# Performance work log

Hardware: AMD Instinct MI355X
Metric: run time of the kernel (lower is better)

The kernel has to match this reference:

```python
import jax, jax.numpy as jnp
import numpy as np

H, DH = 4, 32  # heads, dim_head
EPS = 1e-5


def _split_heads(t, b, n):
    # b n m (h d) -> b h n m d
    return t.reshape(b, n, n, H, DH).transpose(0, 3, 1, 2, 4)


def setup_inputs() -> dict:
    key = jax.random.key(0)
    ks = jax.random.split(key, 8)
    b, n, d = 1, 256, 128
    s = 0.02
    return {
        "edges": jax.random.normal(ks[0], (b, n, n, d), jnp.float32),
        "mask": jax.random.randint(ks[1], (b, n, n), 0, 2) > 0,
        "ln_gamma": jnp.ones((d,), jnp.float32),
        "ln_beta": jnp.zeros((d,), jnp.float32),
        "W_qkv": jax.random.normal(ks[2], (d, 3 * H * DH), jnp.float32) * s,
        "W_b": jax.random.normal(ks[3], (d, H), jnp.float32) * s,
        "W_g": jax.random.normal(ks[4], (d, H * DH), jnp.float32) * s,
        "b_g": jnp.zeros((H * DH,), jnp.float32),
        "W_out": jax.random.normal(ks[5], (H * DH, d), jnp.float32) * s,
        "b_out": jnp.zeros((d,), jnp.float32),
    }


def reference(edges, mask, ln_gamma, ln_beta, W_qkv, W_b, W_g, b_g, W_out, b_out):
    b, n = edges.shape[0], edges.shape[1]
    scale = DH ** -0.5
    # pre-norm (LayerNorm over feature dim)
    mu = edges.mean(-1, keepdims=True)
    var = ((edges - mu) ** 2).mean(-1, keepdims=True)
    x = (edges - mu) * jax.lax.rsqrt(var + EPS) * ln_gamma + ln_beta

    qkv = x @ W_qkv
    q, k, v = jnp.split(qkv, 3, axis=-1)
    q, k, v = (_split_heads(t, b, n) for t in (q, k, v))  # b h i j d
    g = _split_heads(jax.nn.sigmoid(x @ W_g + b_g), b, n)  # b h i j d
    bias = (x @ W_b).transpose(0, 3, 1, 2)  # b h j k

    # starting-node attention: keys/values share row i
    sim = jnp.einsum("bhijd,bhikd->bhijk", q, k) * scale + bias[:, :, None, :, :]
    neg = jnp.finfo(sim.dtype).min
    am = (~mask)[:, None, :, :, None]  # b 1 i j 1
    sim = jnp.where(am, neg, sim)
    g = jnp.where(am, neg, g)
    attn = jax.nn.softmax(sim, axis=-1)
    out = g * jnp.einsum("bhijk,bhikd->bhijd", attn, v)
    # b h i j d -> b i j (h d)
    out = out.transpose(0, 2, 3, 1, 4).reshape(b, n, n, H * DH)
    return out @ W_out + b_out
```

## Files before the change

kernel.cpp:

```cpp
#include <hip/hip_runtime.h>
#include <hip/hip_bf16.h>
#include <hip/hip_fp16.h>


#define NP  256
#define DD  128
#define HSTR 2097152

typedef short bf16x8 __attribute__((ext_vector_type(8)));
typedef float f32x4  __attribute__((ext_vector_type(4)));

__device__ __forceinline__ float bf2f(ushort u) {
    union { unsigned int v; float f; } c; c.v = ((unsigned int)u) << 16; return c.f;
}
__device__ __forceinline__ float asf(unsigned int v) {
    union { unsigned int v; float f; } c; c.v = v; return c.f;
}
__device__ __forceinline__ ushort f2bf(float f) {
    union { float f; unsigned int v; } c; c.f = f;
    unsigned int x = c.v;
    return (ushort)((x + 0x7FFFu + ((x >> 16) & 1u)) >> 16);
}
__device__ __forceinline__ unsigned int packbf(float a, float b) {
    __hip_bfloat162 t = __float22bfloat162_rn(make_float2(a, b));
    union { __hip_bfloat162 h; unsigned int u; } c; c.h = t; return c.u;
}
__device__ __forceinline__ f32x4 mfma16(bf16x8 a, bf16x8 b, f32x4 c) {
    return __builtin_amdgcn_mfma_f32_16x16x32_bf16(a, b, c, 0, 0, 0);
}

#define NEGV (-3.4028234663852886e38f)
#define SCALE 0.17677669529663687f

__global__ __launch_bounds__(256) void k_wconv(
    const float* __restrict__ Wqkv, const float* __restrict__ Wg,
    const float* __restrict__ Wout, const float* __restrict__ Wb,
    ushort* __restrict__ WT, ushort* __restrict__ WoT,
    ushort* __restrict__ WbT16)
{
    int idx = blockIdx.x * 256 + threadIdx.x;
    if (idx < 65536) {
        int n = idx >> 7, k = idx & 127;
        float v = (n < 384) ? Wqkv[(size_t)k * 384 + n]
                            : Wg[(size_t)k * 128 + (n - 384)];
        WT[idx] = f2bf(v);
    } else if (idx < 81920) {
        int i2 = idx - 65536;
        int c = i2 >> 7, e = i2 & 127;
        WoT[i2] = f2bf(Wout[(size_t)e * 128 + c]);
    } else {
        int i3 = idx - 81920;
        int c = i3 >> 7, e = i3 & 127;
        WbT16[i3] = (c < 4) ? f2bf(Wb[(size_t)e * 4 + c]) : (ushort)0;
    }
}

__global__ __launch_bounds__(256) void k_lnqkvg(
    const float* __restrict__ edges, const float* __restrict__ gamma,
    const float* __restrict__ beta,  const ushort* __restrict__ WbT16,
    const ushort* __restrict__ WT,   const float* __restrict__ bg,
    ushort* __restrict__ Bo16,
    ushort* __restrict__ Qo, ushort* __restrict__ Ko,
    ushort* __restrict__ Vo, ushort* __restrict__ Go)
{
    __shared__ __align__(16) ushort As[64][136];
    __shared__ __align__(16) ushort Bs[128][136];
    const int tid = threadIdx.x, w = tid >> 6, lane = tid & 63;
    const int lr = lane & 15, lg = lane >> 4;
    const int wm = w >> 1, wn = w & 1;
    const int p0 = blockIdx.x * 64;
    const f32x4 zz = {0.f, 0.f, 0.f, 0.f};

    {
        const int row = w * 16 + lr;
        const int part = lg;
        const float* ep = edges + (size_t)(p0 + row) * DD + part * 32;
        float4 xv[8];
        #pragma unroll
        for (int t = 0; t < 8; ++t)
            xv[t] = *reinterpret_cast<const float4*>(ep + t * 4);
        float s = 0.f, ss = 0.f;
        #pragma unroll
        for (int t = 0; t < 8; ++t) {
            s  += (xv[t].x + xv[t].y) + (xv[t].z + xv[t].w);
            ss += (xv[t].x * xv[t].x + xv[t].y * xv[t].y)
                + (xv[t].z * xv[t].z + xv[t].w * xv[t].w);
        }
        s  += __shfl_xor(s, 16);  s  += __shfl_xor(s, 32);
        ss += __shfl_xor(ss, 16); ss += __shfl_xor(ss, 32);
        const float mu = s * 0.0078125f;
        const float var = ss * 0.0078125f - mu * mu;
        const float rstd = rsqrtf(var + 1e-5f);
        const float* gp = gamma + part * 32;
        const float* bp = beta + part * 32;
        #pragma unroll
        for (int u = 0; u < 4; ++u) {
            float4 a = xv[2 * u], b = xv[2 * u + 1];
            float4 ga = *reinterpret_cast<const float4*>(gp + u * 8);
            float4 gb = *reinterpret_cast<const float4*>(gp + u * 8 + 4);
            float4 ba = *reinterpret_cast<const float4*>(bp + u * 8);
            float4 bb = *reinterpret_cast<const float4*>(bp + u * 8 + 4);
            float cg;
            uint4 st;
            float v0, v1;
            cg = rstd * ga.x; v0 = a.x * cg + (ba.x - mu * cg);
            cg = rstd * ga.y; v1 = a.y * cg + (ba.y - mu * cg);
            st.x = packbf(v0, v1);
            cg = rstd * ga.z; v0 = a.z * cg + (ba.z - mu * cg);
            cg = rstd * ga.w; v1 = a.w * cg + (ba.w - mu * cg);
            st.y = packbf(v0, v1);
            cg = rstd * gb.x; v0 = b.x * cg + (bb.x - mu * cg);
            cg = rstd * gb.y; v1 = b.y * cg + (bb.y - mu * cg);
            st.z = packbf(v0, v1);
            cg = rstd * gb.z; v0 = b.z * cg + (bb.z - mu * cg);
            cg = rstd * gb.w; v1 = b.w * cg + (bb.w - mu * cg);
            st.w = packbf(v0, v1);
            *reinterpret_cast<uint4*>(&As[row][part * 32 + u * 8]) = st;
        }
    }
    {
        f32x4 bacc = zz;
        #pragma unroll
        for (int kk = 0; kk < 4; ++kk) {
            bf16x8 wb = *reinterpret_cast<const bf16x8*>(&WbT16[(size_t)lr * DD + kk * 32 + lg * 8]);
            bf16x8 xf = *reinterpret_cast<const bf16x8*>(&As[w * 16 + lr][kk * 32 + lg * 8]);
            bacc = mfma16(wb, xf, bacc);
        }
        if (lg == 0) {
            const int p = p0 + w * 16 + lr;
            const int j = p >> 8, k = p & 255;
            const int fn = k >> 4, lgk = (k >> 2) & 3, rr = k & 3;
            const size_t fo = (((size_t)j * 4 + lgk) * 16 + fn) * 4 + rr;
            #pragma unroll
            for (int r = 0; r < 4; ++r)
                Bo16[(size_t)r * 65536 + fo] = f2bf(bacc[r]);
        }
    }

    for (int seg = 0; seg < 4; ++seg) {
        const int n0 = seg * 128;
        __syncthreads();
        #pragma unroll
        for (int it = 0; it < 8; ++it) {
            int idx = it * 256 + tid;
            int r = idx >> 4, c = (idx & 15) * 8;
            *reinterpret_cast<uint4*>(&Bs[r][c]) =
                *reinterpret_cast<const uint4*>(&WT[(size_t)(n0 + r) * DD + c]);
        }
        __syncthreads();
        f32x4 acc[2][4];
        #pragma unroll
        for (int m = 0; m < 2; ++m)
            #pragma unroll
            for (int n = 0; n < 4; ++n) acc[m][n] = zz;
        #pragma unroll
        for (int kk = 0; kk < 4; ++kk) {
            bf16x8 a0 = *reinterpret_cast<const bf16x8*>(&As[wm * 32 + lr][kk * 32 + lg * 8]);
            bf16x8 a1 = *reinterpret_cast<const bf16x8*>(&As[wm * 32 + 16 + lr][kk * 32 + lg * 8]);
            #pragma unroll
            for (int n = 0; n < 4; ++n) {
                bf16x8 b = *reinterpret_cast<const bf16x8*>(&Bs[wn * 64 + n * 16 + lr][kk * 32 + lg * 8]);
                acc[0][n] = mfma16(b, a0, acc[0][n]);
                acc[1][n] = mfma16(b, a1, acc[1][n]);
            }
        }
        #pragma unroll
        for (int n = 0; n < 4; ++n) {
            const int ccb = wn * 64 + n * 16 + 4 * lg;
            const int hh = (wn * 64 + n * 16) >> 5;
            const int dhb = ccb & 31;
            float4 bg4;
            if (seg == 3) bg4 = *reinterpret_cast<const float4*>(&bg[ccb]);
            #pragma unroll
            for (int m = 0; m < 2; ++m) {
                const int p = p0 + wm * 32 + m * 16 + lr;
                const size_t off = (size_t)hh * HSTR + (size_t)p * 32 + dhb;
                float v0 = acc[m][n][0], v1 = acc[m][n][1];
                float v2 = acc[m][n][2], v3 = acc[m][n][3];
                uint2 st;
                if (seg == 0) {
                    st.x = packbf(v0 * SCALE, v1 * SCALE);
                    st.y = packbf(v2 * SCALE, v3 * SCALE);
                    *reinterpret_cast<uint2*>(&Qo[off]) = st;
                } else if (seg == 1) {
                    st.x = packbf(v0, v1); st.y = packbf(v2, v3);
                    *reinterpret_cast<uint2*>(&Ko[off]) = st;
                } else if (seg == 2) {
                    st.x = packbf(v0, v1); st.y = packbf(v2, v3);
                    *reinterpret_cast<uint2*>(&Vo[off]) = st;
                } else {
                    float s0 = 1.0f / (1.0f + __expf(-(v0 + bg4.x)));
                    float s1 = 1.0f / (1.0f + __expf(-(v1 + bg4.y)));
                    float s2 = 1.0f / (1.0f + __expf(-(v2 + bg4.z)));
                    float s3 = 1.0f / (1.0f + __expf(-(v3 + bg4.w)));
                    st.x = packbf(s0, s1); st.y = packbf(s2, s3);
                    *reinterpret_cast<uint2*>(&Go[off]) = st;
                }
            }
        }
    }
}

__global__ __launch_bounds__(256, 2) void k_attn9(
    const ushort* __restrict__ Qw, const ushort* __restrict__ Kw,
    const ushort* __restrict__ Vw, const ushort* __restrict__ Bo16,
    const int* __restrict__ mask, ushort* __restrict__ OPre)
{
    __shared__ __align__(16) ushort Ks[256][40];
    __shared__ __align__(16) ushort Vt[32][268];
    const int tid = threadIdx.x, w = tid >> 6, lane = tid & 63;
    const int lr = lane & 15, lg = lane >> 4;
    const int bid = blockIdx.x;
    const int h = (bid & 7) >> 1;
    const int i = ((bid >> 3) << 1) | (bid & 1);
    const int ib = i * NP;
    const size_t base = (size_t)h * HSTR + (size_t)ib * 32;

    #pragma unroll
    for (int it = 0; it < 4; ++it) {
        int idx = it * 256 + tid;
        int r = idx >> 2, c = (idx & 3) * 8;
        *reinterpret_cast<uint4*>(&Ks[r][c]) =
            *reinterpret_cast<const uint4*>(&Kw[base + (size_t)r * 32 + c]);
    }
    #pragma unroll
    for (int it = 0; it < 8; ++it) {
        int idx = it * 256 + tid;
        int d = idx & 31, k4 = (idx >> 5) * 4;
        int kk4 = (k4 & ~31) | (((k4 >> 2) & 1) << 4) | (((k4 >> 3) & 3) << 2);
        ushort4 v;
        v.x = Vw[base + (size_t)(kk4 + 0) * 32 + d];
        v.y = Vw[base + (size_t)(kk4 + 1) * 32 + d];
        v.z = Vw[base + (size_t)(kk4 + 2) * 32 + d];
        v.w = Vw[base + (size_t)(kk4 + 3) * 32 + d];
        *reinterpret_cast<ushort4*>(&Vt[d][k4]) = v;
    }
    __syncthreads();

    const ushort* bias_h = Bo16 + (size_t)h * 65536;
    const f32x4 zz = {0.f, 0.f, 0.f, 0.f};

    for (int jt = 0; jt < 4; ++jt) {
        const int jb = jt * 64 + w * 16;
        const int jq = jb + lr;
        bf16x8 q = *reinterpret_cast<const bf16x8*>(&Qw[base + (size_t)jq * 32 + lg * 8]);
        const ushort* bp = bias_h + ((size_t)jq * 4 + lg) * 64;
        f32x4 s[16];
        #pragma unroll
        for (int u = 0; u < 8; ++u) {
            uint4 b4 = *reinterpret_cast<const uint4*>(bp + u * 8);
            f32x4 s0, s1;
            s0[0] = asf(b4.x << 16); s0[1] = asf(b4.x & 0xffff0000u);
            s0[2] = asf(b4.y << 16); s0[3] = asf(b4.y & 0xffff0000u);
            s1[0] = asf(b4.z << 16); s1[1] = asf(b4.z & 0xffff0000u);
            s1[2] = asf(b4.w << 16); s1[3] = asf(b4.w & 0xffff0000u);
            s[2 * u] = s0; s[2 * u + 1] = s1;
        }
        #pragma unroll
        for (int fn = 0; fn < 16; ++fn) {
            bf16x8 a = *reinterpret_cast<const bf16x8*>(&Ks[fn * 16 + lr][lg * 8]);
            s[fn] = mfma16(a, q, s[fn]);
        }
        float mx = -3.402823466e38f;
        #pragma unroll
        for (int fn = 0; fn < 16; ++fn) {
            float m01 = fmaxf(s[fn][0], s[fn][1]);
            float m23 = fmaxf(s[fn][2], s[fn][3]);
            mx = fmaxf(mx, fmaxf(m01, m23));
        }
        mx = fmaxf(mx, __shfl_xor(mx, 16));
        mx = fmaxf(mx, __shfl_xor(mx, 32));
        float sum = 0.f;
        #pragma unroll
        for (int fn = 0; fn < 16; ++fn) {
            #pragma unroll
            for (int r = 0; r < 4; ++r) {
                float e = __expf(s[fn][r] - mx);
                s[fn][r] = e; sum += e;
            }
        }
        sum += __shfl_xor(sum, 16);
        sum += __shfl_xor(sum, 32);
        const bool masked = (mask[ib + jq] == 0);
        const float iv = masked ? 1.0f : (1.0f / sum);

        f32x4 o0 = zz, o1 = zz;
        #pragma unroll
        for (int m = 0; m < 8; ++m) {
            union { unsigned int u[4]; bf16x8 v; } pa;
            pa.u[0] = masked ? 0x3B803B80u : packbf(s[2 * m][0], s[2 * m][1]);
            pa.u[1] = masked ? 0x3B803B80u : packbf(s[2 * m][2], s[2 * m][3]);
            pa.u[2] = masked ? 0x3B803B80u : packbf(s[2 * m + 1][0], s[2 * m + 1][1]);
            pa.u[3] = masked ? 0x3B803B80u : packbf(s[2 * m + 1][2], s[2 * m + 1][3]);
            bf16x8 v0 = *reinterpret_cast<const bf16x8*>(&Vt[lr][m * 32 + lg * 8]);
            bf16x8 v1 = *reinterpret_cast<const bf16x8*>(&Vt[16 + lr][m * 32 + lg * 8]);
            o0 = mfma16(v0, pa.v, o0);
            o1 = mfma16(v1, pa.v, o1);
        }
        const size_t off = base + (size_t)jq * 32;
        uint2 u0, u1;
        u0.x = packbf(o0[0] * iv, o0[1] * iv);
        u0.y = packbf(o0[2] * iv, o0[3] * iv);
        u1.x = packbf(o1[0] * iv, o1[1] * iv);
        u1.y = packbf(o1[2] * iv, o1[3] * iv);
        *reinterpret_cast<uint2*>(&OPre[off + 4 * lg])      = u0;
        *reinterpret_cast<uint2*>(&OPre[off + 16 + 4 * lg]) = u1;
    }
}

__device__ __forceinline__ unsigned int gate2(unsigned int o2, unsigned int g2, bool mk) {
    float a0 = bf2f((ushort)(o2 & 0xffffu)), a1 = bf2f((ushort)(o2 >> 16));
    float g0 = mk ? NEGV : bf2f((ushort)(g2 & 0xffffu));
    float g1 = mk ? NEGV : bf2f((ushort)(g2 >> 16));
    return packbf(a0 * g0, a1 * g1);
}

__global__ __launch_bounds__(256) void k_gemm_out(
    const ushort* __restrict__ OPre, const ushort* __restrict__ Gw,
    const int* __restrict__ mask, const ushort* __restrict__ WoT,
    const float* __restrict__ bout, float* __restrict__ out)
{
    __shared__ __align__(16) ushort As[64][136];
    __shared__ __align__(16) ushort Bs[128][136];
    const int tid = threadIdx.x;
    const int p0 = blockIdx.x * 64;
    #pragma unroll
    for (int it = 0; it < 4; ++it) {
        int idx = it * 256 + tid;
        int r = idx >> 4, c = (idx & 15) * 8;
        int hh = c >> 5, dq = c & 31;
        const int p = p0 + r;
        const size_t go = (size_t)hh * HSTR + (size_t)p * 32 + dq;
        uint4 ov = *reinterpret_cast<const uint4*>(&OPre[go]);
        uint4 gv = *reinterpret_cast<const uint4*>(&Gw[go]);
        const bool mk = (mask[p] == 0);
        uint4 rs;
        rs.x = gate2(ov.x, gv.x, mk);
        rs.y = gate2(ov.y, gv.y, mk);
        rs.z = gate2(ov.z, gv.z, mk);
        rs.w = gate2(ov.w, gv.w, mk);
        *reinterpret_cast<uint4*>(&As[r][c]) = rs;
    }
    #pragma unroll
    for (int it = 0; it < 8; ++it) {
        int idx = it * 256 + tid;
        int r = idx >> 4, c = (idx & 15) * 8;
        *reinterpret_cast<uint4*>(&Bs[r][c]) =
            *reinterpret_cast<const uint4*>(&WoT[(size_t)r * DD + c]);
    }
    __syncthreads();
    const int w = tid >> 6, lane = tid & 63;
    const int wm = w >> 1, wn = w & 1;
    const int lr = lane & 15, lg = lane >> 4;
    const f32x4 zz = {0.f, 0.f, 0.f, 0.f};
    f32x4 acc[2][4];
    #pragma unroll
    for (int m = 0; m < 2; ++m)
        #pragma unroll
        for (int n = 0; n < 4; ++n) acc[m][n] = zz;
    #pragma unroll
    for (int kk = 0; kk < 4; ++kk) {
        bf16x8 a0 = *reinterpret_cast<const bf16x8*>(&As[wm * 32 + lr][kk * 32 + lg * 8]);
        bf16x8 a1 = *reinterpret_cast<const bf16x8*>(&As[wm * 32 + 16 + lr][kk * 32 + lg * 8]);
        #pragma unroll
        for (int n = 0; n < 4; ++n) {
            bf16x8 b = *reinterpret_cast<const bf16x8*>(&Bs[wn * 64 + n * 16 + lr][kk * 32 + lg * 8]);
            acc[0][n] = mfma16(b, a0, acc[0][n]);
            acc[1][n] = mfma16(b, a1, acc[1][n]);
        }
    }
    #pragma unroll
    for (int n = 0; n < 4; ++n) {
        const int cb = wn * 64 + n * 16 + 4 * lg;
        const float4 bo4 = *reinterpret_cast<const float4*>(&bout[cb]);
        #pragma unroll
        for (int m = 0; m < 2; ++m) {
            const int p = p0 + wm * 32 + m * 16 + lr;
            float4 st;
            st.x = acc[m][n][0] + bo4.x;
            st.y = acc[m][n][1] + bo4.y;
            st.z = acc[m][n][2] + bo4.z;
            st.w = acc[m][n][3] + bo4.w;
            *reinterpret_cast<float4*>(&out[(size_t)p * DD + cb]) = st;
        }
    }
}

extern "C" void kernel_launch(void* const* d_in, const int* in_sizes, int n_in,
                              void* d_out, int out_size, void* d_ws, size_t ws_size,
                              hipStream_t stream) {
    const float* edges = (const float*)d_in[0];
    const int*   mask  = (const int*)d_in[1];
    const float* gamma = (const float*)d_in[2];
    const float* beta  = (const float*)d_in[3];
    const float* Wqkv  = (const float*)d_in[4];
    const float* Wb    = (const float*)d_in[5];
    const float* Wg    = (const float*)d_in[6];
    const float* bg    = (const float*)d_in[7];
    const float* Wout  = (const float*)d_in[8];
    const float* bout  = (const float*)d_in[9];
    float* out = (float*)d_out;

    char* ws = (char*)d_ws;
    ushort* OPre = (ushort*)(ws);
    ushort* Qw  = (ushort*)(ws + 1u * 16777216u);
    ushort* Kw  = (ushort*)(ws + 2u * 16777216u);
    ushort* Vw  = (ushort*)(ws + 3u * 16777216u);
    ushort* Gw  = (ushort*)(ws + 4u * 16777216u);
    ushort* Bo16 = (ushort*)(ws + 5u * 16777216u);
    ushort* WT  = (ushort*)(ws + 5u * 16777216u + 524288u);
    ushort* WoT = (ushort*)(ws + 5u * 16777216u + 524288u + 131072u);
    ushort* WbT16 = (ushort*)(ws + 5u * 16777216u + 524288u + 131072u + 32768u);

    k_wconv<<<dim3(328), dim3(256), 0, stream>>>(Wqkv, Wg, Wout, Wb, WT, WoT, WbT16);
    k_lnqkvg<<<dim3(1024), dim3(256), 0, stream>>>(edges, gamma, beta, WbT16, WT, bg,
                                                   Bo16, Qw, Kw, Vw, Gw);
    k_attn9<<<dim3(1024), dim3(256), 0, stream>>>(Qw, Kw, Vw, Bo16, mask, OPre);
    k_gemm_out<<<dim3(1024), dim3(256), 0, stream>>>(OPre, Gw, mask, WoT, bout, out);
}
```

Measured before the change: 92.10 us.

## Fuse gating into attention kernel and widen attention blocks to 512 threads

Moves the sigmoid-gate multiply and mask handling from the output GEMM's A-tile load into the attention epilogue. The GEMM then reads the already-gated attention output directly, dropping a full read of the gate tensor and the mask there. The attention kernel now uses 512-thread blocks with 8 waves, fewer loop iterations and a simpler block-to-(head,row) mapping. This adds gate loads and register pressure to the attention kernel and changes occupancy bounds.

```diff
diff --git a/kernel.cpp b/kernel.cpp
--- a/kernel.cpp
+++ b/kernel.cpp
@@ -201,9 +201,10 @@
     }
 }
 
-__global__ __launch_bounds__(256, 2) void k_attn9(
+__global__ __launch_bounds__(512, 4) void k_attn10(
     const ushort* __restrict__ Qw, const ushort* __restrict__ Kw,
-    const ushort* __restrict__ Vw, const ushort* __restrict__ Bo16,
+    const ushort* __restrict__ Vw, const ushort* __restrict__ Gw,
+    const ushort* __restrict__ Bo16,
     const int* __restrict__ mask, ushort* __restrict__ OPre)
 {
     __shared__ __align__(16) ushort Ks[256][40];
@@ -211,21 +212,21 @@
     const int tid = threadIdx.x, w = tid >> 6, lane = tid & 63;
     const int lr = lane & 15, lg = lane >> 4;
     const int bid = blockIdx.x;
-    const int h = (bid & 7) >> 1;
-    const int i = ((bid >> 3) << 1) | (bid & 1);
+    const int h = bid & 3;
+    const int i = bid >> 2;
     const int ib = i * NP;
     const size_t base = (size_t)h * HSTR + (size_t)ib * 32;
 
     #pragma unroll
-    for (int it = 0; it < 4; ++it) {
-        int idx = it * 256 + tid;
+    for (int it = 0; it < 2; ++it) {
+        int idx = it * 512 + tid;
         int r = idx >> 2, c = (idx & 3) * 8;
         *reinterpret_cast<uint4*>(&Ks[r][c]) =
             *reinterpret_cast<const uint4*>(&Kw[base + (size_t)r * 32 + c]);
     }
     #pragma unroll
-    for (int it = 0; it < 8; ++it) {
-        int idx = it * 256 + tid;
+    for (int it = 0; it < 4; ++it) {
+        int idx = it * 512 + tid;
         int d = idx & 31, k4 = (idx >> 5) * 4;
         int kk4 = (k4 & ~31) | (((k4 >> 2) & 1) << 4) | (((k4 >> 3) & 3) << 2);
         ushort4 v;
@@ -240,8 +241,9 @@
     const ushort* bias_h = Bo16 + (size_t)h * 65536;
     const f32x4 zz = {0.f, 0.f, 0.f, 0.f};
 
-    for (int jt = 0; jt < 4; ++jt) {
-        const int jb = jt * 64 + w * 16;
+    #pragma unroll
+    for (int jt = 0; jt < 2; ++jt) {
+        const int jb = jt * 128 + w * 16;
         const int jq = jb + lr;
         bf16x8 q = *reinterpret_cast<const bf16x8*>(&Qw[base + (size_t)jq * 32 + lg * 8]);
         const ushort* bp = bias_h + ((size_t)jq * 4 + lg) * 64;
@@ -298,26 +300,28 @@
             o1 = mfma16(v1, pa.v, o1);
         }
         const size_t off = base + (size_t)jq * 32;
+        uint2 gv0 = *reinterpret_cast<const uint2*>(&Gw[off + 4 * lg]);
+        uint2 gv1 = *reinterpret_cast<const uint2*>(&Gw[off + 16 + 4 * lg]);
+        float g0 = masked ? NEGV : bf2f((ushort)(gv0.x & 0xffffu));
+        float g1 = masked ? NEGV : bf2f((ushort)(gv0.x >> 16));
+        float g2 = masked ? NEGV : bf2f((ushort)(gv0.y & 0xffffu));
+        float g3 = masked ? NEGV : bf2f((ushort)(gv0.y >> 16));
+        float g4 = masked ? NEGV : bf2f((ushort)(gv1.x & 0xffffu));
+        float g5 = masked ? NEGV : bf2f((ushort)(gv1.x >> 16));
+        float g6 = masked ? NEGV : bf2f((ushort)(gv1.y & 0xffffu));
+        float g7 = masked ? NEGV : bf2f((ushort)(gv1.y >> 16));
         uint2 u0, u1;
-        u0.x = packbf(o0[0] * iv, o0[1] * iv);
-        u0.y = packbf(o0[2] * iv, o0[3] * iv);
-        u1.x = packbf(o1[0] * iv, o1[1] * iv);
-        u1.y = packbf(o1[2] * iv, o1[3] * iv);
+        u0.x = packbf(o0[0] * iv * g0, o0[1] * iv * g1);
+        u0.y = packbf(o0[2] * iv * g2, o0[3] * iv * g3);
+        u1.x = packbf(o1[0] * iv * g4, o1[1] * iv * g5);
+        u1.y = packbf(o1[2] * iv * g6, o1[3] * iv * g7);
         *reinterpret_cast<uint2*>(&OPre[off + 4 * lg])      = u0;
         *reinterpret_cast<uint2*>(&OPre[off + 16 + 4 * lg]) = u1;
     }
 }
 
-__device__ __forceinline__ unsigned int gate2(unsigned int o2, unsigned int g2, bool mk) {
-    float a0 = bf2f((ushort)(o2 & 0xffffu)), a1 = bf2f((ushort)(o2 >> 16));
-    float g0 = mk ? NEGV : bf2f((ushort)(g2 & 0xffffu));
-    float g1 = mk ? NEGV : bf2f((ushort)(g2 >> 16));
-    return packbf(a0 * g0, a1 * g1);
-}
-
 __global__ __launch_bounds__(256) void k_gemm_out(
-    const ushort* __restrict__ OPre, const ushort* __restrict__ Gw,
-    const int* __restrict__ mask, const ushort* __restrict__ WoT,
+    const ushort* __restrict__ OPre, const ushort* __restrict__ WoT,
     const float* __restrict__ bout, float* __restrict__ out)
 {
     __shared__ __align__(16) ushort As[64][136];
@@ -331,15 +335,8 @@
         int hh = c >> 5, dq = c & 31;
         const int p = p0 + r;
         const size_t go = (size_t)hh * HSTR + (size_t)p * 32 + dq;
-        uint4 ov = *reinterpret_cast<const uint4*>(&OPre[go]);
-        uint4 gv = *reinterpret_cast<const uint4*>(&Gw[go]);
-        const bool mk = (mask[p] == 0);
-        uint4 rs;
-        rs.x = gate2(ov.x, gv.x, mk);
-        rs.y = gate2(ov.y, gv.y, mk);
-        rs.z = gate2(ov.z, gv.z, mk);
-        rs.w = gate2(ov.w, gv.w, mk);
-        *reinterpret_cast<uint4*>(&As[r][c]) = rs;
+        *reinterpret_cast<uint4*>(&As[r][c]) =
+            *reinterpret_cast<const uint4*>(&OPre[go]);
     }
     #pragma unroll
     for (int it = 0; it < 8; ++it) {
@@ -415,6 +412,6 @@
     k_wconv<<<dim3(328), dim3(256), 0, stream>>>(Wqkv, Wg, Wout, Wb, WT, WoT, WbT16);
     k_lnqkvg<<<dim3(1024), dim3(256), 0, stream>>>(edges, gamma, beta, WbT16, WT, bg,
                                                    Bo16, Qw, Kw, Vw, Gw);
-    k_attn9<<<dim3(1024), dim3(256), 0, stream>>>(Qw, Kw, Vw, Bo16, mask, OPre);
-    k_gemm_out<<<dim3(1024), dim3(256), 0, stream>>>(OPre, Gw, mask, WoT, bout, out);
-}
+    k_attn10<<<dim3(1024), dim3(512), 0, stream>>>(Qw, Kw, Vw, Gw, Bo16, mask, OPre);
+    k_gemm_out<<<dim3(1024), dim3(256), 0, stream>>>(OPre, WoT, bout, out);
+}
```

After: 87.83 us. -4.6%, faster.
